# Kernel optimization log

Measured on AMD Instinct MI355X. Metric: run time of the kernel, lower is better.

The kernel has to match this reference:

```python
import jax, jax.numpy as jnp
import numpy as np

B, S, H, V, E = 64, 20, 128, 50257, 300


def gru(p, x, h):
    # tf.contrib.rnn.GRUCell: r,u = sigmoid([x,h]@Wg + bg); c = tanh([x, r*h]@Wc + bc); h' = u*h + (1-u)*c
    gk, gb, ck, cb = p
    xh = jnp.concatenate([x, h], axis=-1)
    r, u = jnp.split(jax.nn.sigmoid(xh @ gk + gb), 2, axis=-1)
    c = jnp.tanh(jnp.concatenate([x, r * h], axis=-1) @ ck + cb)
    return u * h + (1.0 - u) * c


def setup_inputs() -> dict:
    key = jax.random.key(0)
    ks = jax.random.split(key, 32)
    s = 0.08
    rn = lambda k, shp: (jax.random.normal(k, shp, jnp.float32) * s)
    inp = {}
    inp['x'] = jax.random.randint(ks[0], (B, S), 0, V, dtype=jnp.int32)
    inp['x_length'] = jax.random.randint(ks[1], (B,), 1, S + 1, dtype=jnp.int32)
    inp['y'] = jax.random.randint(ks[2], (B, S), 0, V, dtype=jnp.int32)
    inp['y_length'] = jax.random.randint(ks[3], (B,), 1, S + 1, dtype=jnp.int32)
    inp['embedding'] = jax.random.normal(ks[4], (V, E), jnp.float32) * 0.1
    # encoder GRU: layer0 in=E, layer1 in=H
    inp['e0_gk'] = rn(ks[5], (E + H, 2 * H)); inp['e0_gb'] = rn(ks[6], (2 * H,))
    inp['e0_ck'] = rn(ks[7], (E + H, H));     inp['e0_cb'] = rn(ks[8], (H,))
    inp['e1_gk'] = rn(ks[9], (2 * H, 2 * H)); inp['e1_gb'] = rn(ks[10], (2 * H,))
    inp['e1_ck'] = rn(ks[11], (2 * H, H));    inp['e1_cb'] = rn(ks[12], (H,))
    # decoder GRU: layer0 in = E + attention_size(H) = E+H, layer1 in=H
    inp['d0_gk'] = rn(ks[13], (E + 2 * H, 2 * H)); inp['d0_gb'] = rn(ks[14], (2 * H,))
    inp['d0_ck'] = rn(ks[15], (E + 2 * H, H));     inp['d0_cb'] = rn(ks[16], (H,))
    inp['d1_gk'] = rn(ks[17], (2 * H, 2 * H));     inp['d1_gb'] = rn(ks[18], (2 * H,))
    inp['d1_ck'] = rn(ks[19], (2 * H, H));         inp['d1_cb'] = rn(ks[20], (H,))
    # Bahdanau attention (num_units=H) + attention output layer + vocab projection
    inp['W_mem'] = rn(ks[21], (H, H))
    inp['W_q'] = rn(ks[22], (H, H))
    inp['v_att'] = rn(ks[23], (H,))
    inp['W_attn'] = rn(ks[24], (2 * H, H))
    inp['W_proj'] = rn(ks[25], (H, V))
    inp['b_proj'] = jnp.zeros((V,), jnp.float32)
    return inp


def _forward(x, x_length, y, y_length, embedding,
             e0_gk, e0_gb, e0_ck, e0_cb, e1_gk, e1_gb, e1_ck, e1_cb,
             d0_gk, d0_gb, d0_ck, d0_cb, d1_gk, d1_gb, d1_ck, d1_cb,
             W_mem, W_q, v_att, W_attn, W_proj, b_proj):
    e0 = (e0_gk, e0_gb, e0_ck, e0_cb)
    e1 = (e1_gk, e1_gb, e1_ck, e1_cb)
    d0 = (d0_gk, d0_gb, d0_ck, d0_cb)
    d1 = (d1_gk, d1_gb, d1_ck, d1_cb)
    t_idx = jnp.arange(S)
    x_valid = t_idx[None, :] < x_length[:, None]   # [B,S]
    y_valid = t_idx[None, :] < y_length[:, None]   # [B,S]

    # ---- encoder: 2-layer GRU dynamic_rnn with sequence_length semantics ----
    ex = embedding[x]                               # [B,S,E]
    zeros = jnp.zeros((x.shape[0], H), embedding.dtype)

    def enc_step(carry, inp_t):
        h0, h1 = carry
        xt, vt = inp_t                              # xt [B,E], vt [B,1]
        n0 = gru(e0, xt, h0)
        n1 = gru(e1, n0, h1)
        n0 = jnp.where(vt, n0, h0)                  # copy-through past seq end
        n1 = jnp.where(vt, n1, h1)
        return (n0, n1), jnp.where(vt, n1, 0.0)     # outputs zeroed past seq end

    (h0f, h1f), mem = jax.lax.scan(
        enc_step, (zeros, zeros),
        (ex.transpose(1, 0, 2), x_valid.T[:, :, None]))
    memory = mem.transpose(1, 0, 2)                 # [B,S,H] encoder outputs

    # ---- Bahdanau attention precompute ----
    keys = jnp.einsum('bsh,hu->bsu', memory, W_mem)  # memory_layer(memory)
    neg_inf = jnp.finfo(memory.dtype).min

    # ---- attention decoder (TrainingHelper) ----
    ey = embedding[y]                               # [B,S,E]
    attn0 = jnp.zeros((x.shape[0], H), embedding.dtype)

    def dec_step(carry, inp_t):
        h0, h1, attn = carry
        yt, vt = inp_t                              # yt [B,E], vt [B,1]
        ci = jnp.concatenate([yt, attn], axis=-1)   # cell input = [emb, prev attention]
        n0 = gru(d0, ci, h0)
        n1 = gru(d1, n0, h1)
        q = n1 @ W_q                                # query_layer(cell_output)
        sc = jnp.einsum('bsu,u->bs', jnp.tanh(keys + q[:, None, :]), v_att)
        sc = jnp.where(x_valid, sc, neg_inf)        # memory_sequence_length mask
        al = jax.nn.softmax(sc, axis=-1)            # [B,S]
        ctx = jnp.einsum('bs,bsh->bh', al, memory)  # context
        na = jnp.concatenate([n1, ctx], axis=-1) @ W_attn  # attention_layer (no bias)
        logits = na @ W_proj + b_proj               # projection_layer
        logits = jnp.where(vt, logits, 0.0)         # dynamic_decode zeroes finished emits
        return (n0, n1, na), logits

    _, logits = jax.lax.scan(
        dec_step, (h0f, h1f, attn0),
        (ey.transpose(1, 0, 2), y_valid.T[:, :, None]))
    return logits.transpose(1, 0, 2)                # [B,S,V] rnn_output


def reference(x, x_length, y, y_length, embedding,
              e0_gk, e0_gb, e0_ck, e0_cb, e1_gk, e1_gb, e1_ck, e1_cb,
              d0_gk, d0_gb, d0_ck, d0_cb, d1_gk, d1_gb, d1_ck, d1_cb,
              W_mem, W_q, v_att, W_attn, W_proj, b_proj):
    return _forward(x, x_length, y, y_length, embedding,
                    e0_gk, e0_gb, e0_ck, e0_cb, e1_gk, e1_gb, e1_ck, e1_cb,
                    d0_gk, d0_gb, d0_ck, d0_cb, d1_gk, d1_gb, d1_ck, d1_cb,
                    W_mem, W_q, v_att, W_attn, W_proj, b_proj)
```

## Files before the change

### kernel.cpp

```cpp
#include <hip/hip_runtime.h>
#include <hip/hip_bf16.h>
#include <hip/hip_fp16.h>

#define Bb 64
#define Ss 20
#define Hh 128
#define Vv 50257
#define Ee 300
#define Vpad 50304

typedef short bf16x8 __attribute__((ext_vector_type(8)));
typedef float f32x4 __attribute__((ext_vector_type(4)));
typedef _Float16 h16x8 __attribute__((ext_vector_type(8)));

__device__ __forceinline__ unsigned short f2bf(float f){
  unsigned u = __float_as_uint(f);
  u += 0x7fff + ((u >> 16) & 1);
  return (unsigned short)(u >> 16);
}
__device__ __forceinline__ float sigm(float x){ return 1.f / (1.f + __expf(-x)); }
__device__ __forceinline__ float tanh_fast(float x){
  float e = __expf(2.f * x);
  return 1.f - 2.f / (e + 1.f);
}

template<int K4>
__device__ __forceinline__ float dotT(const float* __restrict__ w, const float* v){
  float a0 = 0.f, a1 = 0.f, a2 = 0.f, a3 = 0.f;
  const float4* w4 = (const float4*)w;
  const float4* v4 = (const float4*)v;
#pragma unroll
  for (int i = 0; i < K4; i++){
    float4 wv = w4[i]; float4 xv = v4[i];
    a0 = fmaf(wv.x, xv.x, a0); a1 = fmaf(wv.y, xv.y, a1);
    a2 = fmaf(wv.z, xv.z, a2); a3 = fmaf(wv.w, xv.w, a3);
  }
  return (a0 + a1) + (a2 + a3);
}

template<int K8>
__device__ __forceinline__ float dotH(const _Float16* __restrict__ w, const float* v){
  float a0 = 0.f, a1 = 0.f, a2 = 0.f, a3 = 0.f;
  const h16x8* w8 = (const h16x8*)w;
  const float4* v4 = (const float4*)v;
#pragma unroll
  for (int i = 0; i < K8; i++){
    h16x8 hv = w8[i];
    float4 x0 = v4[2*i], x1 = v4[2*i+1];
    a0 = fmaf((float)hv[0], x0.x, a0); a1 = fmaf((float)hv[1], x0.y, a1);
    a2 = fmaf((float)hv[2], x0.z, a2); a3 = fmaf((float)hv[3], x0.w, a3);
    a0 = fmaf((float)hv[4], x1.x, a0); a1 = fmaf((float)hv[5], x1.y, a1);
    a2 = fmaf((float)hv[6], x1.z, a2); a3 = fmaf((float)hv[7], x1.w, a3);
  }
  return (a0 + a1) + (a2 + a3);
}


struct TMat { const float* src; void* dst; int r0, R, C, h; };
struct TList { TMat m[15]; };

__global__ __launch_bounds__(256) void wtrans_kernel(TList L){
  TMat t = L.m[blockIdx.y];
  int idx = blockIdx.x * 256 + threadIdx.x;
  int total = t.R * t.C;
  if (idx >= total) return;
  int o = idx / t.R;
  int i = idx - o * t.R;
  float val = t.src[(size_t)(t.r0 + i) * t.C + o];
  if (t.h) ((_Float16*)t.dst)[idx] = (_Float16)val;
  else     ((float*)t.dst)[idx]    = val;
}

__global__ __launch_bounds__(256) void wpt_kernel(const float* __restrict__ Wp,
                                                  unsigned short* __restrict__ Wpt){
  __shared__ unsigned short tile[64][136];
  int n0 = blockIdx.x * 64;
  int tid = threadIdx.x;
  for (int idx = tid; idx < 8192; idx += 256){
    int k = idx >> 6, nn = idx & 63;
    int n = n0 + nn;
    float f = (n < Vv) ? Wp[(size_t)k * Vv + n] : 0.f;
    tile[nn][k] = f2bf(f);
  }
  __syncthreads();
  for (int idx = tid; idx < 1024; idx += 256){
    int nn = idx >> 4, c = idx & 15;
    uint4 v = *reinterpret_cast<const uint4*>(&tile[nn][c * 8]);
    *reinterpret_cast<uint4*>(Wpt + (((size_t)(n0 + nn)) << 7) + c * 8) = v;
  }
}


__global__ __launch_bounds__(256) void pre_kernel(
    const int* __restrict__ x, const int* __restrict__ y, const float* __restrict__ emb,
    const float* __restrict__ egx, const float* __restrict__ ecx,
    const float* __restrict__ egb, const float* __restrict__ ecb,
    const float* __restrict__ dgx, const float* __restrict__ dcx,
    const float* __restrict__ dgb, const float* __restrict__ dcb,
    float* __restrict__ epg, float* __restrict__ epc,
    float* __restrict__ dpg, float* __restrict__ dpc)
{
  __shared__ __align__(16) float er[Ee];
  int tid = threadIdx.x, ti = blockIdx.x, which = blockIdx.y;
  int tok = which ? y[ti] : x[ti];
  if (tid < 75)
    ((float4*)er)[tid] = ((const float4*)(emb + (size_t)tok * Ee))[tid];
  __syncthreads();
  const float* gx = which ? dgx : egx;
  const float* cx = which ? dcx : ecx;
  float accg = (which ? dgb : egb)[tid] + dotT<75>(gx + (size_t)tid * Ee, er);
  (which ? dpg : epg)[ti * 256 + tid] = accg;
  if (tid < 128){
    float accc = (which ? dcb : ecb)[tid] + dotT<75>(cx + (size_t)tid * Ee, er);
    (which ? dpc : epc)[ti * 128 + tid] = accc;
  }
}


__global__ __launch_bounds__(256, 1) void recur2(
    const int* __restrict__ xlen,
    const float* __restrict__ epg, const float* __restrict__ epc,
    const float* __restrict__ dpg, const float* __restrict__ dpc,
    const _Float16* __restrict__ e0_gh_h, const _Float16* __restrict__ e0_ch_h,
    const _Float16* __restrict__ e1_g_h, const _Float16* __restrict__ e1_c_h,
    const float* __restrict__ e1_gb,  const float* __restrict__ e1_cb,
    const _Float16* __restrict__ d0_gah_h, const _Float16* __restrict__ d0_cah_h,
    const _Float16* __restrict__ d1_g_h, const _Float16* __restrict__ d1_c_h,
    const float* __restrict__ d1_gb,  const float* __restrict__ d1_cb,
    const _Float16* __restrict__ W_mem_h, const _Float16* __restrict__ W_q_h,
    const _Float16* __restrict__ W_attn_h, const float* __restrict__ v_att,
    unsigned short* __restrict__ na_bf)
{
  __shared__ __align__(16) float mem_s[Ss][Hh];
  __shared__ __align__(16) float keys_s[Ss][132];
  __shared__ __align__(16) float h0[Hh], h1[Hh], attn[Hh], n0[Hh], n1[Hh], rh[Hh], q[Hh], ctx[Hh];
  __shared__ __align__(16) float gates[2*Hh];
  __shared__ __align__(16) float vatt_s[Hh];
  __shared__ float part[Ss][8];

  const int tid = threadIdx.x, b = blockIdx.x;
  if (tid < Hh){ h0[tid] = 0.f; h1[tid] = 0.f; attn[tid] = 0.f; vatt_s[tid] = v_att[tid]; }
  __syncthreads();
  const int xl = xlen[b];
  const int o = tid >> 1, half = tid & 1;

  for (int t = 0; t < Ss; t++){
    const int tix = b * Ss + t;
    {
      float g = epg[(tix << 8) + tid] + dotH<16>(e0_gh_h + tid * 128, h0);
      float sg = sigm(g);
      if (tid < Hh) rh[tid] = sg * h0[tid];
      else          gates[tid] = sg;
    }
    __syncthreads();
    {
      float a = dotH<8>(e0_ch_h + o * 128 + half * 64, rh + half * 64);
      a += __shfl_xor(a, 1);
      if (!half){
        float c = tanh_fast(epc[(tix << 7) + o] + a);
        float u = gates[128 + o];
        n0[o] = u * h0[o] + (1.f - u) * c;
      }
    }
    __syncthreads();
    {
      float g1 = e1_gb[tid] + dotH<16>(e1_g_h + tid * 256, n0)
                            + dotH<16>(e1_g_h + tid * 256 + 128, h1);
      float sg = sigm(g1);
      if (tid < Hh) rh[tid] = sg * h1[tid];
      else          gates[tid] = sg;
    }
    __syncthreads();
    {
      const _Float16* base = e1_c_h + o * 256 + half * 128;
      float a = half ? dotH<16>(base, rh) : dotH<16>(base, n0);
      a += __shfl_xor(a, 1);
      if (!half){
        float c = tanh_fast(e1_cb[o] + a);
        float u = gates[128 + o];
        float nh = u * h1[o] + (1.f - u) * c;
        bool v = (t < xl);
        mem_s[t][o] = v ? nh : 0.f;
        h1[o] = v ? nh : h1[o];
        h0[o] = v ? n0[o] : h0[o];
      }
    }
    __syncthreads();
  }

  for (int idx = tid; idx < Ss * Hh; idx += 256){
    int s = idx >> 7, j = idx & 127;
    keys_s[s][j] = dotH<16>(W_mem_h + j * 128, mem_s[s]);
  }
  __syncthreads();

  for (int t = 0; t < Ss; t++){
    const int tix = b * Ss + t;
    {
      float g = dpg[(tix << 8) + tid] + dotH<16>(d0_gah_h + tid * 256, attn)
                                      + dotH<16>(d0_gah_h + tid * 256 + 128, h0);
      float sg = sigm(g);
      if (tid < Hh) rh[tid] = sg * h0[tid];
      else          gates[tid] = sg;
    }
    __syncthreads();
    {
      const _Float16* base = d0_cah_h + o * 256 + half * 128;
      float a = half ? dotH<16>(base, rh) : dotH<16>(base, attn);
      a += __shfl_xor(a, 1);
      if (!half){
        float c = tanh_fast(dpc[(tix << 7) + o] + a);
        float u = gates[128 + o];
        float nv = u * h0[o] + (1.f - u) * c;
        n0[o] = nv; h0[o] = nv;
      }
    }
    __syncthreads();
    {
      float g1 = d1_gb[tid] + dotH<16>(d1_g_h + tid * 256, n0)
                            + dotH<16>(d1_g_h + tid * 256 + 128, h1);
      float sg = sigm(g1);
      if (tid < Hh) rh[tid] = sg * h1[tid];
      else          gates[tid] = sg;
    }
    __syncthreads();
    {
      const _Float16* base = d1_c_h + o * 256 + half * 128;
      float a = half ? dotH<16>(base, rh) : dotH<16>(base, n0);
      a += __shfl_xor(a, 1);
      if (!half){
        float c = tanh_fast(d1_cb[o] + a);
        float u = gates[128 + o];
        float nh = u * h1[o] + (1.f - u) * c;
        n1[o] = nh; h1[o] = nh;
      }
    }
    __syncthreads();
    {
      float a = dotH<8>(W_q_h + o * 128 + half * 64, n1 + half * 64);
      a += __shfl_xor(a, 1);
      if (!half) q[o] = a;
    }
    __syncthreads();
    if (tid < Ss * 8){
      int s = tid >> 3, p = tid & 7;
      float a = 0.f;
#pragma unroll
      for (int c2 = 0; c2 < 16; c2++){
        int u2 = p * 16 + c2;
        a += tanh_fast(keys_s[s][u2] + q[u2]) * vatt_s[u2];
      }
      part[s][p] = a;
    }
    __syncthreads();
    if (tid < Hh){
      float e_[Ss];
      float mx = -3.4e38f;
#pragma unroll
      for (int s = 0; s < Ss; s++){
        float v = ((part[s][0] + part[s][1]) + (part[s][2] + part[s][3]))
                + ((part[s][4] + part[s][5]) + (part[s][6] + part[s][7]));
        v = (s < xl) ? v : -3.4e38f;
        e_[s] = v; mx = fmaxf(mx, v);
      }
      float sm = 0.f;
#pragma unroll
      for (int s = 0; s < Ss; s++){
        float e = (s < xl) ? __expf(e_[s] - mx) : 0.f;
        e_[s] = e; sm += e;
      }
      float inv = 1.f / sm;
      float a = 0.f;
#pragma unroll
      for (int s = 0; s < Ss; s++) a = fmaf(e_[s], mem_s[s][tid], a);
      ctx[tid] = a * inv;
    }
    __syncthreads();
    {
      const _Float16* base = W_attn_h + o * 256 + half * 128;
      float a = half ? dotH<16>(base, ctx) : dotH<16>(base, n1);
      a += __shfl_xor(a, 1);
      if (!half){
        attn[o] = a;
        na_bf[(tix << 7) + o] = f2bf(a);
      }
    }
    __syncthreads();
  }
}


__global__ __launch_bounds__(256) void proj2(
    const unsigned short* __restrict__ na_bf, const unsigned short* __restrict__ Wpt,
    const float* __restrict__ b_proj, const int* __restrict__ ylen,
    float* __restrict__ out)
{
  __shared__ int yl_s[Bb];
  const int tid = threadIdx.x;
  if (tid < Bb) yl_s[tid] = ylen[tid];
  const int n0 = blockIdx.x * 128, m0 = blockIdx.y * 64;
  const int lane = tid & 63, w = tid >> 6, lm = lane & 15, qq = lane >> 4;

  f32x4 acc[4][2];
#pragma unroll
  for (int mt = 0; mt < 4; mt++){ acc[mt][0] = (f32x4){0,0,0,0}; acc[mt][1] = (f32x4){0,0,0,0}; }

#pragma unroll
  for (int ks = 0; ks < 4; ks++){
    int ko = ks * 32 + qq * 8;
    bf16x8 b0 = *(const bf16x8*)(Wpt + (((size_t)(n0 + w*32 + lm)) << 7) + ko);
    bf16x8 b1 = *(const bf16x8*)(Wpt + (((size_t)(n0 + w*32 + 16 + lm)) << 7) + ko);
#pragma unroll
    for (int mt = 0; mt < 4; mt++){
      bf16x8 a = *(const bf16x8*)(na_bf + (((size_t)(m0 + mt*16 + lm)) << 7) + ko);
      acc[mt][0] = __builtin_amdgcn_mfma_f32_16x16x32_bf16(a, b0, acc[mt][0], 0, 0, 0);
      acc[mt][1] = __builtin_amdgcn_mfma_f32_16x16x32_bf16(a, b1, acc[mt][1], 0, 0, 0);
    }
  }
  __syncthreads();

#pragma unroll
  for (int mt = 0; mt < 4; mt++){
    int row = m0 + mt*16 + qq*4;
#pragma unroll
    for (int n2 = 0; n2 < 2; n2++){
      int col = n0 + w*32 + n2*16 + lm;
      if (col < Vv){
        float bp = b_proj[col];
#pragma unroll
        for (int r = 0; r < 4; r++){
          int rr = row + r;
          int bb = rr / Ss;
          int tt = rr - bb * Ss;
          float val = (tt < yl_s[bb]) ? (acc[mt][n2][r] + bp) : 0.f;
          out[(size_t)rr * Vv + col] = val;
        }
      }
    }
  }
}

extern "C" void kernel_launch(void* const* d_in, const int* in_sizes, int n_in,
                              void* d_out, int out_size, void* d_ws, size_t ws_size,
                              hipStream_t stream) {
  const int*   x        = (const int*)d_in[0];
  const int*   x_length = (const int*)d_in[1];
  const int*   y        = (const int*)d_in[2];
  const int*   y_length = (const int*)d_in[3];
  const float* emb      = (const float*)d_in[4];
  const float* e0_gk = (const float*)d_in[5];  const float* e0_gb = (const float*)d_in[6];
  const float* e0_ck = (const float*)d_in[7];  const float* e0_cb = (const float*)d_in[8];
  const float* e1_gk = (const float*)d_in[9];  const float* e1_gb = (const float*)d_in[10];
  const float* e1_ck = (const float*)d_in[11]; const float* e1_cb = (const float*)d_in[12];
  const float* d0_gk = (const float*)d_in[13]; const float* d0_gb = (const float*)d_in[14];
  const float* d0_ck = (const float*)d_in[15]; const float* d0_cb = (const float*)d_in[16];
  const float* d1_gk = (const float*)d_in[17]; const float* d1_gb = (const float*)d_in[18];
  const float* d1_ck = (const float*)d_in[19]; const float* d1_cb = (const float*)d_in[20];
  const float* W_mem = (const float*)d_in[21]; const float* W_q   = (const float*)d_in[22];
  const float* v_att = (const float*)d_in[23]; const float* W_attn= (const float*)d_in[24];
  const float* W_proj= (const float*)d_in[25]; const float* b_proj= (const float*)d_in[26];
  float* out = (float*)d_out;

  size_t off = 0;
  auto alloc = [&](size_t bytes) -> void* {
    void* p = (char*)d_ws + off;
    off += (bytes + 255) & ~(size_t)255;
    return p;
  };
  unsigned short* Wpt   = (unsigned short*)alloc((size_t)Vpad * 128 * 2);
  unsigned short* na_bf = (unsigned short*)alloc((size_t)Bb * Ss * Hh * 2);
  float* epg = (float*)alloc((size_t)Bb*Ss*256*4);
  float* epc = (float*)alloc((size_t)Bb*Ss*128*4);
  float* dpg = (float*)alloc((size_t)Bb*Ss*256*4);
  float* dpc = (float*)alloc((size_t)Bb*Ss*128*4);
  float* e0_gx_t  = (float*)alloc(256*300*4);
  float* e0_cx_t  = (float*)alloc(128*300*4);
  float* d0_gx_t  = (float*)alloc(256*300*4);
  float* d0_cx_t  = (float*)alloc(128*300*4);
  _Float16* e0_gh_h  = (_Float16*)alloc(256*128*2);
  _Float16* e0_ch_h  = (_Float16*)alloc(128*128*2);
  _Float16* e1_g_h   = (_Float16*)alloc(256*256*2);
  _Float16* e1_c_h   = (_Float16*)alloc(128*256*2);
  _Float16* d0_gah_h = (_Float16*)alloc(256*256*2);
  _Float16* d0_cah_h = (_Float16*)alloc(128*256*2);
  _Float16* d1_g_h   = (_Float16*)alloc(256*256*2);
  _Float16* d1_c_h   = (_Float16*)alloc(128*256*2);
  _Float16* W_mem_h  = (_Float16*)alloc(128*128*2);
  _Float16* W_q_h    = (_Float16*)alloc(128*128*2);
  _Float16* W_attn_h = (_Float16*)alloc(128*256*2);

  TList L;
  L.m[0]  = { e0_gk, e0_gx_t,    0, 300, 256, 0 };
  L.m[1]  = { e0_gk, e0_gh_h,  300, 128, 256, 1 };
  L.m[2]  = { e0_ck, e0_cx_t,    0, 300, 128, 0 };
  L.m[3]  = { e0_ck, e0_ch_h,  300, 128, 128, 1 };
  L.m[4]  = { e1_gk, e1_g_h,     0, 256, 256, 1 };
  L.m[5]  = { e1_ck, e1_c_h,     0, 256, 128, 1 };
  L.m[6]  = { d0_gk, d0_gx_t,    0, 300, 256, 0 };
  L.m[7]  = { d0_gk, d0_gah_h, 300, 256, 256, 1 };
  L.m[8]  = { d0_ck, d0_cx_t,    0, 300, 128, 0 };
  L.m[9]  = { d0_ck, d0_cah_h, 300, 256, 128, 1 };
  L.m[10] = { d1_gk, d1_g_h,     0, 256, 256, 1 };
  L.m[11] = { d1_ck, d1_c_h,     0, 256, 128, 1 };
  L.m[12] = { W_mem, W_mem_h,    0, 128, 128, 1 };
  L.m[13] = { W_q,   W_q_h,      0, 128, 128, 1 };
  L.m[14] = { W_attn,W_attn_h,   0, 256, 128, 1 };

  wtrans_kernel<<<dim3(300, 15), 256, 0, stream>>>(L);
  wpt_kernel<<<Vpad / 64, 256, 0, stream>>>(W_proj, Wpt);
  pre_kernel<<<dim3(Bb * Ss, 2), 256, 0, stream>>>(
      x, y, emb, e0_gx_t, e0_cx_t, e0_gb, e0_cb,
      d0_gx_t, d0_cx_t, d0_gb, d0_cb, epg, epc, dpg, dpc);
  recur2<<<Bb, 256, 0, stream>>>(
      x_length, epg, epc, dpg, dpc,
      e0_gh_h, e0_ch_h, e1_g_h, e1_c_h, e1_gb, e1_cb,
      d0_gah_h, d0_cah_h, d1_g_h, d1_c_h, d1_gb, d1_cb,
      W_mem_h, W_q_h, W_attn_h, v_att, na_bf);
  proj2<<<dim3(Vpad / 128, (Bb * Ss) / 64), 256, 0, stream>>>(
      na_bf, Wpt, b_proj, y_length, out);
}
```

Baseline: 1.461 ms.

## Interleave recurrent weights in fp32 float4 layout for coalesced per-thread dot products

The weight-prep kernel now writes every GRU and attention weight matrix as fp32 in a layout where each group of 4 input rows for one output is a float4, and consecutive outputs are adjacent. In each dot-product step neighbouring threads therefore read neighbouring float4s instead of each thread walking its own contiguous row. The fp16 copies used by the recurrent kernel are replaced by fp32, which removes the half-to-float conversions and the rounding. The cost is twice the weight bytes streamed from cache at every serial timestep.

```diff
diff --git a/kernel.cpp b/kernel.cpp
--- a/kernel.cpp
+++ b/kernel.cpp
@@ -1,6 +1,5 @@
 #include <hip/hip_runtime.h>
 #include <hip/hip_bf16.h>
-#include <hip/hip_fp16.h>
 
 #define Bb 64
 #define Ss 20
@@ -11,7 +10,6 @@
 
 typedef short bf16x8 __attribute__((ext_vector_type(8)));
 typedef float f32x4 __attribute__((ext_vector_type(4)));
-typedef _Float16 h16x8 __attribute__((ext_vector_type(8)));
 
 __device__ __forceinline__ unsigned short f2bf(float f){
   unsigned u = __float_as_uint(f);
@@ -24,39 +22,23 @@
   return 1.f - 2.f / (e + 1.f);
 }
 
-template<int K4>
-__device__ __forceinline__ float dotT(const float* __restrict__ w, const float* v){
+template<int N4, int C>
+__device__ __forceinline__ float dotI(const float* __restrict__ w, int o, const float* v){
   float a0 = 0.f, a1 = 0.f, a2 = 0.f, a3 = 0.f;
   const float4* w4 = (const float4*)w;
   const float4* v4 = (const float4*)v;
 #pragma unroll
-  for (int i = 0; i < K4; i++){
-    float4 wv = w4[i]; float4 xv = v4[i];
+  for (int i = 0; i < N4; i++){
+    float4 wv = w4[(size_t)i * C + o];
+    float4 xv = v4[i];
     a0 = fmaf(wv.x, xv.x, a0); a1 = fmaf(wv.y, xv.y, a1);
     a2 = fmaf(wv.z, xv.z, a2); a3 = fmaf(wv.w, xv.w, a3);
   }
   return (a0 + a1) + (a2 + a3);
 }
 
-template<int K8>
-__device__ __forceinline__ float dotH(const _Float16* __restrict__ w, const float* v){
-  float a0 = 0.f, a1 = 0.f, a2 = 0.f, a3 = 0.f;
-  const h16x8* w8 = (const h16x8*)w;
-  const float4* v4 = (const float4*)v;
-#pragma unroll
-  for (int i = 0; i < K8; i++){
-    h16x8 hv = w8[i];
-    float4 x0 = v4[2*i], x1 = v4[2*i+1];
-    a0 = fmaf((float)hv[0], x0.x, a0); a1 = fmaf((float)hv[1], x0.y, a1);
-    a2 = fmaf((float)hv[2], x0.z, a2); a3 = fmaf((float)hv[3], x0.w, a3);
-    a0 = fmaf((float)hv[4], x1.x, a0); a1 = fmaf((float)hv[5], x1.y, a1);
-    a2 = fmaf((float)hv[6], x1.z, a2); a3 = fmaf((float)hv[7], x1.w, a3);
-  }
-  return (a0 + a1) + (a2 + a3);
-}
-
-
-struct TMat { const float* src; void* dst; int r0, R, C, h; };
+
+struct TMat { const float* src; float* dst; int r0, R, C; };
 struct TList { TMat m[15]; };
 
 __global__ __launch_bounds__(256) void wtrans_kernel(TList L){
@@ -64,11 +46,12 @@
   int idx = blockIdx.x * 256 + threadIdx.x;
   int total = t.R * t.C;
   if (idx >= total) return;
-  int o = idx / t.R;
-  int i = idx - o * t.R;
-  float val = t.src[(size_t)(t.r0 + i) * t.C + o];
-  if (t.h) ((_Float16*)t.dst)[idx] = (_Float16)val;
-  else     ((float*)t.dst)[idx]    = val;
+  int j  = idx & 3;
+  int r2 = idx >> 2;
+  int o  = r2 % t.C;
+  int i4 = r2 / t.C;
+  int k  = i4 * 4 + j;
+  t.dst[idx] = t.src[(size_t)(t.r0 + k) * t.C + o];
 }
 
 __global__ __launch_bounds__(256) void wpt_kernel(const float* __restrict__ Wp,
@@ -108,10 +91,10 @@
   __syncthreads();
   const float* gx = which ? dgx : egx;
   const float* cx = which ? dcx : ecx;
-  float accg = (which ? dgb : egb)[tid] + dotT<75>(gx + (size_t)tid * Ee, er);
+  float accg = (which ? dgb : egb)[tid] + dotI<75, 256>(gx, tid, er);
   (which ? dpg : epg)[ti * 256 + tid] = accg;
   if (tid < 128){
-    float accc = (which ? dcb : ecb)[tid] + dotT<75>(cx + (size_t)tid * Ee, er);
+    float accc = (which ? dcb : ecb)[tid] + dotI<75, 128>(cx, tid, er);
     (which ? dpc : epc)[ti * 128 + tid] = accc;
   }
 }
@@ -121,14 +104,14 @@
     const int* __restrict__ xlen,
     const float* __restrict__ epg, const float* __restrict__ epc,
     const float* __restrict__ dpg, const float* __restrict__ dpc,
-    const _Float16* __restrict__ e0_gh_h, const _Float16* __restrict__ e0_ch_h,
-    const _Float16* __restrict__ e1_g_h, const _Float16* __restrict__ e1_c_h,
+    const float* __restrict__ e0_gh_i, const float* __restrict__ e0_ch_i,
+    const float* __restrict__ e1_g_i, const float* __restrict__ e1_c_i,
     const float* __restrict__ e1_gb,  const float* __restrict__ e1_cb,
-    const _Float16* __restrict__ d0_gah_h, const _Float16* __restrict__ d0_cah_h,
-    const _Float16* __restrict__ d1_g_h, const _Float16* __restrict__ d1_c_h,
+    const float* __restrict__ d0_gah_i, const float* __restrict__ d0_cah_i,
+    const float* __restrict__ d1_g_i, const float* __restrict__ d1_c_i,
     const float* __restrict__ d1_gb,  const float* __restrict__ d1_cb,
-    const _Float16* __restrict__ W_mem_h, const _Float16* __restrict__ W_q_h,
-    const _Float16* __restrict__ W_attn_h, const float* __restrict__ v_att,
+    const float* __restrict__ W_mem_i, const float* __restrict__ W_q_i,
+    const float* __restrict__ W_attn_i, const float* __restrict__ v_att,
     unsigned short* __restrict__ na_bf)
 {
   __shared__ __align__(16) float mem_s[Ss][Hh];
@@ -147,14 +130,14 @@
   for (int t = 0; t < Ss; t++){
     const int tix = b * Ss + t;
     {
-      float g = epg[(tix << 8) + tid] + dotH<16>(e0_gh_h + tid * 128, h0);
+      float g = epg[(tix << 8) + tid] + dotI<32, 256>(e0_gh_i, tid, h0);
       float sg = sigm(g);
       if (tid < Hh) rh[tid] = sg * h0[tid];
       else          gates[tid] = sg;
     }
     __syncthreads();
     {
-      float a = dotH<8>(e0_ch_h + o * 128 + half * 64, rh + half * 64);
+      float a = dotI<16, 128>(e0_ch_i + half * 8192, o, rh + half * 64);
       a += __shfl_xor(a, 1);
       if (!half){
         float c = tanh_fast(epc[(tix << 7) + o] + a);
@@ -164,16 +147,16 @@
     }
     __syncthreads();
     {
-      float g1 = e1_gb[tid] + dotH<16>(e1_g_h + tid * 256, n0)
-                            + dotH<16>(e1_g_h + tid * 256 + 128, h1);
+      float g1 = e1_gb[tid] + dotI<32, 256>(e1_g_i, tid, n0)
+                            + dotI<32, 256>(e1_g_i + 32768, tid, h1);
       float sg = sigm(g1);
       if (tid < Hh) rh[tid] = sg * h1[tid];
       else          gates[tid] = sg;
     }
     __syncthreads();
     {
-      const _Float16* base = e1_c_h + o * 256 + half * 128;
-      float a = half ? dotH<16>(base, rh) : dotH<16>(base, n0);
+      float a = half ? dotI<32, 128>(e1_c_i + 16384, o, rh)
+                     : dotI<32, 128>(e1_c_i, o, n0);
       a += __shfl_xor(a, 1);
       if (!half){
         float c = tanh_fast(e1_cb[o] + a);
@@ -190,23 +173,23 @@
 
   for (int idx = tid; idx < Ss * Hh; idx += 256){
     int s = idx >> 7, j = idx & 127;
-    keys_s[s][j] = dotH<16>(W_mem_h + j * 128, mem_s[s]);
+    keys_s[s][j] = dotI<32, 128>(W_mem_i, j, mem_s[s]);
   }
   __syncthreads();
 
   for (int t = 0; t < Ss; t++){
     const int tix = b * Ss + t;
     {
-      float g = dpg[(tix << 8) + tid] + dotH<16>(d0_gah_h + tid * 256, attn)
-                                      + dotH<16>(d0_gah_h + tid * 256 + 128, h0);
+      float g = dpg[(tix << 8) + tid] + dotI<32, 256>(d0_gah_i, tid, attn)
+                                      + dotI<32, 256>(d0_gah_i + 32768, tid, h0);
       float sg = sigm(g);
       if (tid < Hh) rh[tid] = sg * h0[tid];
       else          gates[tid] = sg;
     }
     __syncthreads();
     {
-      const _Float16* base = d0_cah_h + o * 256 + half * 128;
-      float a = half ? dotH<16>(base, rh) : dotH<16>(base, attn);
+      float a = half ? dotI<32, 128>(d0_cah_i + 16384, o, rh)
+                     : dotI<32, 128>(d0_cah_i, o, attn);
       a += __shfl_xor(a, 1);
       if (!half){
         float c = tanh_fast(dpc[(tix << 7) + o] + a);
@@ -217,16 +200,16 @@
     }
     __syncthreads();
     {
-      float g1 = d1_gb[tid] + dotH<16>(d1_g_h + tid * 256, n0)
-                            + dotH<16>(d1_g_h + tid * 256 + 128, h1);
+      float g1 = d1_gb[tid] + dotI<32, 256>(d1_g_i, tid, n0)
+                            + dotI<32, 256>(d1_g_i + 32768, tid, h1);
       float sg = sigm(g1);
       if (tid < Hh) rh[tid] = sg * h1[tid];
       else          gates[tid] = sg;
     }
     __syncthreads();
     {
-      const _Float16* base = d1_c_h + o * 256 + half * 128;
-      float a = half ? dotH<16>(base, rh) : dotH<16>(base, n0);
+      float a = half ? dotI<32, 128>(d1_c_i + 16384, o, rh)
+                     : dotI<32, 128>(d1_c_i, o, n0);
       a += __shfl_xor(a, 1);
       if (!half){
         float c = tanh_fast(d1_cb[o] + a);
@@ -237,7 +220,7 @@
     }
     __syncthreads();
     {
-      float a = dotH<8>(W_q_h + o * 128 + half * 64, n1 + half * 64);
+      float a = dotI<16, 128>(W_q_i + half * 8192, o, n1 + half * 64);
       a += __shfl_xor(a, 1);
       if (!half) q[o] = a;
     }
@@ -277,8 +260,8 @@
     }
     __syncthreads();
     {
-      const _Float16* base = W_attn_h + o * 256 + half * 128;
-      float a = half ? dotH<16>(base, ctx) : dotH<16>(base, n1);
+      float a = half ? dotI<32, 128>(W_attn_i + 16384, o, ctx)
+                     : dotI<32, 128>(W_attn_i, o, n1);
       a += __shfl_xor(a, 1);
       if (!half){
         attn[o] = a;
@@ -373,49 +356,49 @@
   float* epc = (float*)alloc((size_t)Bb*Ss*128*4);
   float* dpg = (float*)alloc((size_t)Bb*Ss*256*4);
   float* dpc = (float*)alloc((size_t)Bb*Ss*128*4);
-  float* e0_gx_t  = (float*)alloc(256*300*4);
-  float* e0_cx_t  = (float*)alloc(128*300*4);
-  float* d0_gx_t  = (float*)alloc(256*300*4);
-  float* d0_cx_t  = (float*)alloc(128*300*4);
-  _Float16* e0_gh_h  = (_Float16*)alloc(256*128*2);
-  _Float16* e0_ch_h  = (_Float16*)alloc(128*128*2);
-  _Float16* e1_g_h   = (_Float16*)alloc(256*256*2);
-  _Float16* e1_c_h   = (_Float16*)alloc(128*256*2);
-  _Float16* d0_gah_h = (_Float16*)alloc(256*256*2);
-  _Float16* d0_cah_h = (_Float16*)alloc(128*256*2);
-  _Float16* d1_g_h   = (_Float16*)alloc(256*256*2);
-  _Float16* d1_c_h   = (_Float16*)alloc(128*256*2);
-  _Float16* W_mem_h  = (_Float16*)alloc(128*128*2);
-  _Float16* W_q_h    = (_Float16*)alloc(128*128*2);
-  _Float16* W_attn_h = (_Float16*)alloc(128*256*2);
+  float* e0_gx_i  = (float*)alloc(300*256*4);
+  float* e0_gh_i  = (float*)alloc(128*256*4);
+  float* e0_cx_i  = (float*)alloc(300*128*4);
+  float* e0_ch_i  = (float*)alloc(128*128*4);
+  float* e1_g_i   = (float*)alloc(256*256*4);
+  float* e1_c_i   = (float*)alloc(256*128*4);
+  float* d0_gx_i  = (float*)alloc(300*256*4);
+  float* d0_gah_i = (float*)alloc(256*256*4);
+  float* d0_cx_i  = (float*)alloc(300*128*4);
+  float* d0_cah_i = (float*)alloc(256*128*4);
+  float* d1_g_i   = (float*)alloc(256*256*4);
+  float* d1_c_i   = (float*)alloc(256*128*4);
+  float* W_mem_i  = (float*)alloc(128*128*4);
+  float* W_q_i    = (float*)alloc(128*128*4);
+  float* W_attn_i = (float*)alloc(256*128*4);
 
   TList L;
-  L.m[0]  = { e0_gk, e0_gx_t,    0, 300, 256, 0 };
-  L.m[1]  = { e0_gk, e0_gh_h,  300, 128, 256, 1 };
-  L.m[2]  = { e0_ck, e0_cx_t,    0, 300, 128, 0 };
-  L.m[3]  = { e0_ck, e0_ch_h,  300, 128, 128, 1 };
-  L.m[4]  = { e1_gk, e1_g_h,     0, 256, 256, 1 };
-  L.m[5]  = { e1_ck, e1_c_h,     0, 256, 128, 1 };
-  L.m[6]  = { d0_gk, d0_gx_t,    0, 300, 256, 0 };
-  L.m[7]  = { d0_gk, d0_gah_h, 300, 256, 256, 1 };
-  L.m[8]  = { d0_ck, d0_cx_t,    0, 300, 128, 0 };
-  L.m[9]  = { d0_ck, d0_cah_h, 300, 256, 128, 1 };
-  L.m[10] = { d1_gk, d1_g_h,     0, 256, 256, 1 };
-  L.m[11] = { d1_ck, d1_c_h,     0, 256, 128, 1 };
-  L.m[12] = { W_mem, W_mem_h,    0, 128, 128, 1 };
-  L.m[13] = { W_q,   W_q_h,      0, 128, 128, 1 };
-  L.m[14] = { W_attn,W_attn_h,   0, 256, 128, 1 };
+  L.m[0]  = { e0_gk, e0_gx_i,    0, 300, 256 };
+  L.m[1]  = { e0_gk, e0_gh_i,  300, 128, 256 };
+  L.m[2]  = { e0_ck, e0_cx_i,    0, 300, 128 };
+  L.m[3]  = { e0_ck, e0_ch_i,  300, 128, 128 };
+  L.m[4]  = { e1_gk, e1_g_i,     0, 256, 256 };
+  L.m[5]  = { e1_ck, e1_c_i,     0, 256, 128 };
+  L.m[6]  = { d0_gk, d0_gx_i,    0, 300, 256 };
+  L.m[7]  = { d0_gk, d0_gah_i, 300, 256, 256 };
+  L.m[8]  = { d0_ck, d0_cx_i,    0, 300, 128 };
+  L.m[9]  = { d0_ck, d0_cah_i, 300, 256, 128 };
+  L.m[10] = { d1_gk, d1_g_i,     0, 256, 256 };
+  L.m[11] = { d1_ck, d1_c_i,     0, 256, 128 };
+  L.m[12] = { W_mem, W_mem_i,    0, 128, 128 };
+  L.m[13] = { W_q,   W_q_i,      0, 128, 128 };
+  L.m[14] = { W_attn,W_attn_i,   0, 256, 128 };
 
   wtrans_kernel<<<dim3(300, 15), 256, 0, stream>>>(L);
   wpt_kernel<<<Vpad / 64, 256, 0, stream>>>(W_proj, Wpt);
   pre_kernel<<<dim3(Bb * Ss, 2), 256, 0, stream>>>(
-      x, y, emb, e0_gx_t, e0_cx_t, e0_gb, e0_cb,
-      d0_gx_t, d0_cx_t, d0_gb, d0_cb, epg, epc, dpg, dpc);
+      x, y, emb, e0_gx_i, e0_cx_i, e0_gb, e0_cb,
+      d0_gx_i, d0_cx_i, d0_gb, d0_cb, epg, epc, dpg, dpc);
   recur2<<<Bb, 256, 0, stream>>>(
       x_length, epg, epc, dpg, dpc,
-      e0_gh_h, e0_ch_h, e1_g_h, e1_c_h, e1_gb, e1_cb,
-      d0_gah_h, d0_cah_h, d1_g_h, d1_c_h, d1_gb, d1_cb,
-      W_mem_h, W_q_h, W_attn_h, v_att, na_bf);
+      e0_gh_i, e0_ch_i, e1_g_i, e1_c_i, e1_gb, e1_cb,
+      d0_gah_i, d0_cah_i, d1_g_i, d1_c_i, d1_gb, d1_cb,
+      W_mem_i, W_q_i, W_attn_i, v_att, na_bf);
   proj2<<<dim3(Vpad / 128, (Bb * Ss) / 64), 256, 0, stream>>>(
       na_bf, Wpt, b_proj, y_length, out);
 }
```

Measured after the change: 2.268 ms. +55.2%, slower.
